# Optimization experiments

Measured on AMD Instinct MI355X. Metric: run time of the kernel, lower is better.

## Reference

```python
import jax, jax.numpy as jnp
import numpy as np

V, D, H, L, E = 50000, 512, 512, 4, 40000


def setup_inputs() -> dict:
    key = jax.random.key(0)
    k1, k2, k3 = jax.random.split(key, 3)
    node_embeddings = jax.random.normal(k1, (V, D), dtype=jnp.float32)
    adjacency = jax.random.randint(k2, (L, E, 2), 0, V, dtype=jnp.int32)
    W = jax.random.normal(k3, (L, D, H), dtype=jnp.float32) * (1.0 / np.sqrt(D))
    return {"node_embeddings": node_embeddings, "adjacency": adjacency, "W": W}


def reference(node_embeddings, adjacency, W):
    # adjacency: [L, E, 2] with [:, :, 0] = source node, [:, :, 1] = target node
    src = adjacency[..., 0]  # [L, E]
    tgt = adjacency[..., 1]  # [L, E]
    # Gather source states per edge and apply per-edge-type linear message fn.
    # edge_source_states: [L, E, D]; messages: [L, E, H]
    messages = jnp.einsum("led,ldh->leh", node_embeddings[src], W)
    # Scatter-aggregate (sum) all messages to their target nodes.
    num_nodes = node_embeddings.shape[0]
    aggregated = jax.ops.segment_sum(
        messages.reshape(-1, messages.shape[-1]),  # [L*E, H]
        tgt.reshape(-1),
        num_segments=num_nodes,
    )  # [V, H]
    # message_activation_before_aggregation = False -> activation after aggregation
    return jax.nn.relu(aggregated)
```

## Files before the change

kernel.cpp:

```cpp
#include <hip/hip_runtime.h>
#include <hip/hip_bf16.h>

#define NV 50000
#define VP2 50176
#define ND 512
#define NH 512
#define NL 4
#define NE 40000
#define CAP 16
#define KTOT 2048
#define NKT 32
#define NWG3 1568

typedef short bf16x8 __attribute__((ext_vector_type(8)));
typedef float f32x4  __attribute__((ext_vector_type(4)));

__device__ __forceinline__ unsigned short f2bf(float f) {
    unsigned int u = __float_as_uint(f);
    u += 0x7FFFu + ((u >> 16) & 1u);
    return (unsigned short)(u >> 16);
}
__device__ __forceinline__ unsigned pack_bf2(float x, float y) {
    return (unsigned)f2bf(x) | ((unsigned)f2bf(y) << 16);
}

#define GLL16(gp, lp) __builtin_amdgcn_global_load_lds( \
    (const __attribute__((address_space(1))) void*)(gp), \
    (__attribute__((address_space(3))) void*)(lp), 16, 0, 0)

__global__ void wt2_kernel(const float* __restrict__ W, unsigned short* __restrict__ Wt2) {
    int idx = blockIdx.x * 256 + threadIdx.x;
    int l = idx >> 18;
    int r = idx & 262143;
    int k = r >> 9;
    int h = r & 511;
    Wt2[((size_t)h << 11) + (l << 9) + k] = f2bf(W[idx]);
}

__global__ void place_kernel(const int* __restrict__ adj, int* __restrict__ cnt,
                             int* __restrict__ list) {
    int i = blockIdx.x * 256 + threadIdx.x;
    int2 p = ((const int2*)adj)[i];
    int l = i / NE;
    int cell = p.y * NL + l;
    int pos = atomicAdd(&cnt[cell], 1);
    if (pos < CAP) list[cell * CAP + pos] = p.x;
}

__global__ void __launch_bounds__(256)
agg_pull(const float* __restrict__ emb, const int* __restrict__ cnt,
         const int* __restrict__ list, unsigned* __restrict__ agg2) {
    const int wid  = blockIdx.x * 4 + (threadIdx.x >> 6);
    const int lane = threadIdx.x & 63;
    const int t    = wid >> 2;
    const int l    = wid & 3;
    const int cell = wid;
    const size_t dst = (size_t)t * 1024 + l * 256 + lane;

    int n = cnt[cell]; if (n > CAP) n = CAP;
    const int* lst = list + cell * CAP;

    float2 s0 = {0.f,0.f}, s1 = {0.f,0.f}, s2 = {0.f,0.f}, s3 = {0.f,0.f};
    int j = 0;
    for (; j + 2 <= n; j += 2) {
        const float2* p0 = (const float2*)(emb + (size_t)lst[j]     * ND) + lane;
        const float2* p1 = (const float2*)(emb + (size_t)lst[j + 1] * ND) + lane;
        float2 a0 = p0[0], a1 = p0[64], a2 = p0[128], a3 = p0[192];
        float2 b0 = p1[0], b1 = p1[64], b2 = p1[128], b3 = p1[192];
        s0.x += a0.x + b0.x; s0.y += a0.y + b0.y;
        s1.x += a1.x + b1.x; s1.y += a1.y + b1.y;
        s2.x += a2.x + b2.x; s2.y += a2.y + b2.y;
        s3.x += a3.x + b3.x; s3.y += a3.y + b3.y;
    }
    if (j < n) {
        const float2* p0 = (const float2*)(emb + (size_t)lst[j] * ND) + lane;
        float2 a0 = p0[0], a1 = p0[64], a2 = p0[128], a3 = p0[192];
        s0.x += a0.x; s0.y += a0.y;  s1.x += a1.x; s1.y += a1.y;
        s2.x += a2.x; s2.y += a2.y;  s3.x += a3.x; s3.y += a3.y;
    }
    agg2[dst]       = pack_bf2(s0.x, s0.y);
    agg2[dst + 64]  = pack_bf2(s1.x, s1.y);
    agg2[dst + 128] = pack_bf2(s2.x, s2.y);
    agg2[dst + 192] = pack_bf2(s3.x, s3.y);
}

__device__ __forceinline__ void stage_ab(
    int kt, int t0, int n0, int wave, int lane,
    const unsigned short* __restrict__ agg2, const unsigned short* __restrict__ Wt2,
    unsigned short* sa0, unsigned short* sa1,
    unsigned short* sb0, unsigned short* sb1) {
    const int rowin = lane >> 3;
    const int slt   = lane & 7;
    unsigned short* sa = (kt & 1) ? sa1 : sa0;
    unsigned short* sb = (kt & 1) ? sb1 : sb0;
    const int ko = kt * 64;
#pragma unroll
    for (int r = 0; r < 4; ++r) {
        const int rb  = r * 32 + wave * 8;
        const int row = rb + rowin;
        const unsigned short* srcA = agg2
            + (size_t)(t0 + row) * KTOT + ko + ((slt ^ (row & 7)) << 3);
        const unsigned short* srcB = Wt2
            + (size_t)(n0 + row) * KTOT + ko + ((slt ^ (row & 7)) << 3);
        GLL16(srcA, sa + rb * 64);
        GLL16(srcB, sb + rb * 64);
    }
}

template<bool STG>
__device__ __forceinline__ void tile_step(
    int kt, int t0, int n0, int wave, int lane, int wm, int wn,
    const unsigned short* __restrict__ agg2, const unsigned short* __restrict__ Wt2,
    unsigned short* sa0, unsigned short* sa1,
    unsigned short* sb0, unsigned short* sb1,
    f32x4 (&acc)[4][4]) {
    const int laneL = lane & 15, laneH = lane >> 4;
    const int ax = laneL & 7;
    const unsigned short* pa = (kt & 1) ? sa1 : sa0;
    const unsigned short* pb = (kt & 1) ? sb1 : sb0;

    if (STG) stage_ab(kt + 1, t0, n0, wave, lane, agg2, Wt2, sa0, sa1, sb0, sb1);

    bf16x8 aF[4][2], bF[4][2];
#pragma unroll
    for (int ni = 0; ni < 4; ++ni)
#pragma unroll
        for (int ks = 0; ks < 2; ++ks) {
            const int row = wn * 64 + ni * 16 + laneL;
            bF[ni][ks] = *(const bf16x8*)(pb + row * 64 + (((ks * 4 + laneH) ^ ax) << 3));
        }
#pragma unroll
    for (int mi = 0; mi < 4; ++mi)
#pragma unroll
        for (int ks = 0; ks < 2; ++ks) {
            const int row = wm * 64 + mi * 16 + laneL;
            aF[mi][ks] = *(const bf16x8*)(pa + row * 64 + (((ks * 4 + laneH) ^ ax) << 3));
        }
#pragma unroll
    for (int mi = 0; mi < 4; ++mi)
#pragma unroll
        for (int ni = 0; ni < 4; ++ni)
#pragma unroll
            for (int ks = 0; ks < 2; ++ks)
                acc[mi][ni] = __builtin_amdgcn_mfma_f32_16x16x32_bf16(aF[mi][ks], bF[ni][ks], acc[mi][ni], 0, 0, 0);

    __syncthreads();
}

__global__ void __launch_bounds__(256)
gemm128(const unsigned short* __restrict__ agg2,
        const unsigned short* __restrict__ Wt2,
        float* __restrict__ out) {
    __shared__ unsigned short s_a[2][128 * 64];
    __shared__ unsigned short s_b[2][128 * 64];

    const int orig = blockIdx.x;
    const int wgid = (orig & 7) * (NWG3 / 8) + (orig >> 3);
    const int mt = wgid >> 2, nt = wgid & 3;
    const int t0 = mt * 128, n0 = nt * 128;

    const int tid  = threadIdx.x;
    const int lane = tid & 63;
    const int wave = tid >> 6;
    const int wm   = wave >> 1;
    const int wn   = wave & 1;
    const int laneL = lane & 15, laneH = lane >> 4;

    f32x4 acc[4][4];
#pragma unroll
    for (int mi = 0; mi < 4; ++mi)
#pragma unroll
        for (int ni = 0; ni < 4; ++ni)
            acc[mi][ni] = (f32x4){0.f, 0.f, 0.f, 0.f};

    unsigned short* sa0 = &s_a[0][0]; unsigned short* sa1 = &s_a[1][0];
    unsigned short* sb0 = &s_b[0][0]; unsigned short* sb1 = &s_b[1][0];

    stage_ab(0, t0, n0, wave, lane, agg2, Wt2, sa0, sa1, sb0, sb1);
    __syncthreads();

    for (int kt = 0; kt < NKT - 1; ++kt)
        tile_step<true>(kt, t0, n0, wave, lane, wm, wn, agg2, Wt2, sa0, sa1, sb0, sb1, acc);
    tile_step<false>(NKT - 1, t0, n0, wave, lane, wm, wn, agg2, Wt2, sa0, sa1, sb0, sb1, acc);

#pragma unroll
    for (int mi = 0; mi < 4; ++mi) {
#pragma unroll
        for (int i = 0; i < 4; ++i) {
            int t = t0 + wm * 64 + mi * 16 + laneH * 4 + i;
            if (t < NV) {
#pragma unroll
                for (int ni = 0; ni < 4; ++ni) {
                    int h = n0 + wn * 64 + ni * 16 + laneL;
                    out[(size_t)t * NH + h] = fmaxf(acc[mi][ni][i], 0.f);
                }
            }
        }
    }
}

__global__ void wt_legacy(const float* __restrict__ W, unsigned short* __restrict__ Wt) {
    int idx = blockIdx.x * 256 + threadIdx.x;
    int l = idx >> 18;
    int r = idx & 262143;
    int k = r >> 9;
    int h = r & 511;
    Wt[(l << 18) + (h << 9) + k] = f2bf(W[idx]);
}
__global__ void __launch_bounds__(256)
legacy_msg(const float* __restrict__ emb, const int* __restrict__ adj,
           const unsigned short* __restrict__ Wt, float* __restrict__ out) {
    __shared__ bf16x8 s_a[32 * 64];
    __shared__ int s_src[32];
    __shared__ int s_tgt[32];
    const int bx = blockIdx.x;
    const int l = bx / (NE / 32);
    const int ebase = (bx % (NE / 32)) * 32;
    const int tid = threadIdx.x, lane = tid & 63, wave = tid >> 6;
    if (tid < 32) {
        int2 p = *(const int2*)(adj + ((size_t)l * NE + ebase + tid) * 2);
        s_src[tid] = p.x; s_tgt[tid] = p.y;
    }
    __syncthreads();
    {
        const int r = tid >> 3, part = tid & 7, k0 = part * 64, rxx = r & 7;
        const float* g = emb + (size_t)s_src[r] * ND + k0;
#pragma unroll
        for (int j = 0; j < 8; ++j) {
            float4 f0 = *(const float4*)(g + j * 8);
            float4 f1 = *(const float4*)(g + j * 8 + 4);
            bf16x8 v;
            v[0]=(short)f2bf(f0.x); v[1]=(short)f2bf(f0.y);
            v[2]=(short)f2bf(f0.z); v[3]=(short)f2bf(f0.w);
            v[4]=(short)f2bf(f1.x); v[5]=(short)f2bf(f1.y);
            v[6]=(short)f2bf(f1.z); v[7]=(short)f2bf(f1.w);
            int slot = (k0 >> 3) + j;
            s_a[r * 64 + (slot ^ rxx)] = v;
        }
    }
    __syncthreads();
    const int c0 = wave * 128, laneL = lane & 15, laneH = lane >> 4, arx = laneL & 7;
    f32x4 acc[2][8];
#pragma unroll
    for (int mf = 0; mf < 2; ++mf)
#pragma unroll
        for (int nf = 0; nf < 8; ++nf) acc[mf][nf] = (f32x4){0.f,0.f,0.f,0.f};
    const bf16x8* wb = (const bf16x8*)(Wt + ((size_t)l << 18));
#pragma unroll
    for (int kc = 0; kc < 16; ++kc) {
        int slot = kc * 4 + laneH;
        bf16x8 a0 = s_a[laneL * 64 + (slot ^ arx)];
        bf16x8 a1 = s_a[(16 + laneL) * 64 + (slot ^ arx)];
#pragma unroll
        for (int nf = 0; nf < 8; ++nf) {
            bf16x8 b = wb[(c0 + nf * 16 + laneL) * 64 + slot];
            acc[0][nf] = __builtin_amdgcn_mfma_f32_16x16x32_bf16(a0, b, acc[0][nf], 0, 0, 0);
            acc[1][nf] = __builtin_amdgcn_mfma_f32_16x16x32_bf16(a1, b, acc[1][nf], 0, 0, 0);
        }
    }
#pragma unroll
    for (int mf = 0; mf < 2; ++mf)
#pragma unroll
        for (int nf = 0; nf < 8; ++nf) {
            int h = c0 + nf * 16 + laneL;
#pragma unroll
            for (int i = 0; i < 4; ++i) {
                int er = mf * 16 + laneH * 4 + i;
                atomicAdd(out + (size_t)s_tgt[er] * NH + h, acc[mf][nf][i]);
            }
        }
}
__global__ void legacy_relu(float* __restrict__ o, int n4) {
    int stride = gridDim.x * blockDim.x;
    for (int i = blockIdx.x * blockDim.x + threadIdx.x; i < n4; i += stride) {
        float4 v = ((float4*)o)[i];
        v.x = fmaxf(v.x, 0.f); v.y = fmaxf(v.y, 0.f);
        v.z = fmaxf(v.z, 0.f); v.w = fmaxf(v.w, 0.f);
        ((float4*)o)[i] = v;
    }
}

extern "C" void kernel_launch(void* const* d_in, const int* in_sizes, int n_in,
                              void* d_out, int out_size, void* d_ws, size_t ws_size,
                              hipStream_t stream) {
    const float* emb = (const float*)d_in[0];
    const int*   adj = (const int*)d_in[1];
    const float* W   = (const float*)d_in[2];
    float* out = (float*)d_out;
    char* ws = (char*)d_ws;

    unsigned short* Wt2  = (unsigned short*)ws;
    int*            cnt  = (int*)(ws + 2621440);
    int*            list = (int*)(ws + 3670016);
    unsigned short* agg2 = (unsigned short*)(ws + (16u << 20));

    const size_t need = (16u << 20) + (size_t)VP2 * KTOT * 2;

    if (ws_size >= need) {
        hipMemsetAsync(cnt, 0, (size_t)VP2 * NL * sizeof(int), stream);
        wt2_kernel<<<(NL * ND * NH) / 256, 256, 0, stream>>>(W, Wt2);
        place_kernel<<<(NL * NE) / 256, 256, 0, stream>>>(adj, cnt, list);
        agg_pull<<<(VP2 * NL) / 4, 256, 0, stream>>>(emb, cnt, list, (unsigned*)agg2);
        gemm128<<<NWG3, 256, 0, stream>>>(agg2, Wt2, out);
    } else {
        hipMemsetAsync(d_out, 0, (size_t)out_size * sizeof(float), stream);
        wt_legacy<<<(NL * ND * NH) / 256, 256, 0, stream>>>(W, Wt2);
        legacy_msg<<<NL * (NE / 32), 256, 0, stream>>>(emb, adj, Wt2, out);
        legacy_relu<<<2048, 256, 0, stream>>>(out, out_size / 4);
    }
}
```

Before: 299.2 us.

## Retile GEMM to 256x128 blocks with 512 threads and 32-wide K steps

Replaces the 128x128, 256-thread GEMM with a 256x128 tile run by 8 waves. Each k step is 32 wide, so there are 64 steps, with a new XOR swizzle and a manually double-buffered loop. The larger M tile halves the number of workgroups and the W traffic per output, and smaller K steps cut LDS use per block so more blocks can be resident. In exchange there are twice as many barriers per K, and launch_bounds(512,4) may put pressure on registers.

```diff
diff --git a/kernel.cpp b/kernel.cpp
--- a/kernel.cpp
+++ b/kernel.cpp
@@ -9,8 +9,8 @@
 #define NE 40000
 #define CAP 16
 #define KTOT 2048
-#define NKT 32
-#define NWG3 1568
+#define NKT 64
+#define NWG4 784
 
 typedef short bf16x8 __attribute__((ext_vector_type(8)));
 typedef float f32x4  __attribute__((ext_vector_type(4)));
@@ -84,80 +84,17 @@
     agg2[dst + 192] = pack_bf2(s3.x, s3.y);
 }
 
-__device__ __forceinline__ void stage_ab(
-    int kt, int t0, int n0, int wave, int lane,
-    const unsigned short* __restrict__ agg2, const unsigned short* __restrict__ Wt2,
-    unsigned short* sa0, unsigned short* sa1,
-    unsigned short* sb0, unsigned short* sb1) {
-    const int rowin = lane >> 3;
-    const int slt   = lane & 7;
-    unsigned short* sa = (kt & 1) ? sa1 : sa0;
-    unsigned short* sb = (kt & 1) ? sb1 : sb0;
-    const int ko = kt * 64;
-#pragma unroll
-    for (int r = 0; r < 4; ++r) {
-        const int rb  = r * 32 + wave * 8;
-        const int row = rb + rowin;
-        const unsigned short* srcA = agg2
-            + (size_t)(t0 + row) * KTOT + ko + ((slt ^ (row & 7)) << 3);
-        const unsigned short* srcB = Wt2
-            + (size_t)(n0 + row) * KTOT + ko + ((slt ^ (row & 7)) << 3);
-        GLL16(srcA, sa + rb * 64);
-        GLL16(srcB, sb + rb * 64);
-    }
-}
-
-template<bool STG>
-__device__ __forceinline__ void tile_step(
-    int kt, int t0, int n0, int wave, int lane, int wm, int wn,
-    const unsigned short* __restrict__ agg2, const unsigned short* __restrict__ Wt2,
-    unsigned short* sa0, unsigned short* sa1,
-    unsigned short* sb0, unsigned short* sb1,
-    f32x4 (&acc)[4][4]) {
-    const int laneL = lane & 15, laneH = lane >> 4;
-    const int ax = laneL & 7;
-    const unsigned short* pa = (kt & 1) ? sa1 : sa0;
-    const unsigned short* pb = (kt & 1) ? sb1 : sb0;
-
-    if (STG) stage_ab(kt + 1, t0, n0, wave, lane, agg2, Wt2, sa0, sa1, sb0, sb1);
-
-    bf16x8 aF[4][2], bF[4][2];
-#pragma unroll
-    for (int ni = 0; ni < 4; ++ni)
-#pragma unroll
-        for (int ks = 0; ks < 2; ++ks) {
-            const int row = wn * 64 + ni * 16 + laneL;
-            bF[ni][ks] = *(const bf16x8*)(pb + row * 64 + (((ks * 4 + laneH) ^ ax) << 3));
-        }
-#pragma unroll
-    for (int mi = 0; mi < 4; ++mi)
-#pragma unroll
-        for (int ks = 0; ks < 2; ++ks) {
-            const int row = wm * 64 + mi * 16 + laneL;
-            aF[mi][ks] = *(const bf16x8*)(pa + row * 64 + (((ks * 4 + laneH) ^ ax) << 3));
-        }
-#pragma unroll
-    for (int mi = 0; mi < 4; ++mi)
-#pragma unroll
-        for (int ni = 0; ni < 4; ++ni)
-#pragma unroll
-            for (int ks = 0; ks < 2; ++ks)
-                acc[mi][ni] = __builtin_amdgcn_mfma_f32_16x16x32_bf16(aF[mi][ks], bF[ni][ks], acc[mi][ni], 0, 0, 0);
-
-    __syncthreads();
-}
-
-__global__ void __launch_bounds__(256)
-gemm128(const unsigned short* __restrict__ agg2,
-        const unsigned short* __restrict__ Wt2,
-        float* __restrict__ out) {
-    __shared__ unsigned short s_a[2][128 * 64];
-    __shared__ unsigned short s_b[2][128 * 64];
+__global__ void __launch_bounds__(512, 4)
+gemm32(const unsigned short* __restrict__ agg2,
+       const unsigned short* __restrict__ Wt2,
+       float* __restrict__ out) {
+    __shared__ unsigned short s_a[2 * 256 * 32];
+    __shared__ unsigned short s_b[2 * 128 * 32];
 
     const int orig = blockIdx.x;
-    const int wgid = (orig & 7) * (NWG3 / 8) + (orig >> 3);
+    const int wgid = (orig & 7) * (NWG4 / 8) + (orig >> 3);
     const int mt = wgid >> 2, nt = wgid & 3;
-    const int t0 = mt * 128, n0 = nt * 128;
+    const int t0 = mt * 256, n0 = nt * 128;
 
     const int tid  = threadIdx.x;
     const int lane = tid & 63;
@@ -166,6 +103,19 @@
     const int wn   = wave & 1;
     const int laneL = lane & 15, laneH = lane >> 4;
 
+    const int rowin = lane >> 2;
+    const int sx    = (lane & 3) ^ (rowin & 3) ^ ((rowin >> 2) & 3);
+    const unsigned short* srcA0 = agg2 + (size_t)(t0 + (wave * 2 + 0) * 16 + rowin) * KTOT + sx * 8;
+    const unsigned short* srcA1 = agg2 + (size_t)(t0 + (wave * 2 + 1) * 16 + rowin) * KTOT + sx * 8;
+    const unsigned short* srcB  = Wt2  + (size_t)(n0 + wave * 16 + rowin) * KTOT + sx * 8;
+    const int ldsA0 = (wave * 2 + 0) * 512 + lane * 8;
+    const int ldsA1 = (wave * 2 + 1) * 512 + lane * 8;
+    const int ldsB  = wave * 512 + lane * 8;
+
+    const int rx = (laneL & 3) ^ (laneL >> 2);
+    const int fa = (wm * 64 + laneL) * 32 + ((laneH ^ rx) << 3);
+    const int fb = (wn * 64 + laneL) * 32 + ((laneH ^ rx) << 3);
+
     f32x4 acc[4][4];
 #pragma unroll
     for (int mi = 0; mi < 4; ++mi)
@@ -173,15 +123,40 @@
         for (int ni = 0; ni < 4; ++ni)
             acc[mi][ni] = (f32x4){0.f, 0.f, 0.f, 0.f};
 
-    unsigned short* sa0 = &s_a[0][0]; unsigned short* sa1 = &s_a[1][0];
-    unsigned short* sb0 = &s_b[0][0]; unsigned short* sb1 = &s_b[1][0];
-
-    stage_ab(0, t0, n0, wave, lane, agg2, Wt2, sa0, sa1, sb0, sb1);
+#define STAGE_T(P) do { \
+    GLL16(srcA0, s_a + (P) * 8192 + ldsA0); \
+    GLL16(srcA1, s_a + (P) * 8192 + ldsA1); \
+    GLL16(srcB,  s_b + (P) * 4096 + ldsB);  \
+    srcA0 += 32; srcA1 += 32; srcB += 32; } while (0)
+
+#define COMPUTE_T(P) do { \
+    const unsigned short* pa = s_a + (P) * 8192; \
+    const unsigned short* pb = s_b + (P) * 4096; \
+    bf16x8 aF[4], bF[4]; \
+    _Pragma("unroll") \
+    for (int ni = 0; ni < 4; ++ni) bF[ni] = *(const bf16x8*)(pb + fb + ni * 512); \
+    _Pragma("unroll") \
+    for (int mi = 0; mi < 4; ++mi) aF[mi] = *(const bf16x8*)(pa + fa + mi * 512); \
+    _Pragma("unroll") \
+    for (int mi = 0; mi < 4; ++mi) \
+        _Pragma("unroll") \
+        for (int ni = 0; ni < 4; ++ni) \
+            acc[mi][ni] = __builtin_amdgcn_mfma_f32_16x16x32_bf16(aF[mi], bF[ni], acc[mi][ni], 0, 0, 0); \
+    } while (0)
+
+    STAGE_T(0);
     __syncthreads();
 
-    for (int kt = 0; kt < NKT - 1; ++kt)
-        tile_step<true>(kt, t0, n0, wave, lane, wm, wn, agg2, Wt2, sa0, sa1, sb0, sb1, acc);
-    tile_step<false>(NKT - 1, t0, n0, wave, lane, wm, wn, agg2, Wt2, sa0, sa1, sb0, sb1, acc);
+#pragma unroll 1
+    for (int it = 0; it < 31; ++it) {
+        STAGE_T(1); COMPUTE_T(0); __syncthreads();
+        STAGE_T(0); COMPUTE_T(1); __syncthreads();
+    }
+    STAGE_T(1); COMPUTE_T(0); __syncthreads();
+    COMPUTE_T(1);
+
+#undef STAGE_T
+#undef COMPUTE_T
 
 #pragma unroll
     for (int mi = 0; mi < 4; ++mi) {
@@ -301,7 +276,7 @@
         wt2_kernel<<<(NL * ND * NH) / 256, 256, 0, stream>>>(W, Wt2);
         place_kernel<<<(NL * NE) / 256, 256, 0, stream>>>(adj, cnt, list);
         agg_pull<<<(VP2 * NL) / 4, 256, 0, stream>>>(emb, cnt, list, (unsigned*)agg2);
-        gemm128<<<NWG3, 256, 0, stream>>>(agg2, Wt2, out);
+        gemm32<<<NWG4, 512, 0, stream>>>(agg2, Wt2, out);
     } else {
         hipMemsetAsync(d_out, 0, (size_t)out_size * sizeof(float), stream);
         wt_legacy<<<(NL * ND * NH) / 256, 256, 0, stream>>>(W, Wt2);
```

Measured after the change: 321.4 us. +7.4%, slower.
